# Performance work log

Hardware: AMD Instinct MI355X
Metric: run time of the kernel (lower is better)

The kernel has to match this reference:

```python
import jax, jax.numpy as jnp
import numpy as np

N, E, D, H = 50000, 500000, 128, 4
FH = D // H  # per-head dim of gat1
NEG_SLOPE = 0.2
EPS = 1e-16  # PyG softmax denominator epsilon


def _gat_layer(x, src, dst, W, a_src, a_dst, bias, heads, fh):
    # W: [D_in, heads*fh]; a_src/a_dst: [heads, fh]; bias: [heads*fh]
    n = x.shape[0]
    xp = (x @ W).reshape(n, heads, fh)                     # [N,H,F]
    alpha_s = jnp.einsum('nhf,hf->nh', xp, a_src)          # [N,H]
    alpha_d = jnp.einsum('nhf,hf->nh', xp, a_dst)
    e = alpha_s[src] + alpha_d[dst]                        # [E,H]
    e = jnp.where(e > 0, e, NEG_SLOPE * e)                 # leaky_relu
    # edge softmax grouped by destination node
    m = jax.lax.stop_gradient(jax.ops.segment_max(e, dst, num_segments=n))
    a = jnp.exp(e - m[dst])
    denom = jax.ops.segment_sum(a, dst, num_segments=n)
    a = a / (denom[dst] + EPS)                             # [E,H]
    msg = a[:, :, None] * xp[src]                          # [E,H,F]
    out = jax.ops.segment_sum(msg, dst, num_segments=n)    # [N,H,F]
    return out.reshape(n, heads * fh) + bias


def setup_inputs() -> dict:
    key = jax.random.key(0)
    ks = jax.random.split(key, 20)

    def glorot(k, shape):
        fan_in, fan_out = shape[0], shape[-1]
        std = (2.0 / (fan_in + fan_out)) ** 0.5
        return std * jax.random.normal(k, shape, dtype=jnp.float32)

    inp = {
        'x': jax.random.normal(ks[0], (N, 1), dtype=jnp.float32),
        'edge_index': jax.random.randint(ks[1], (E, 2), 0, N, dtype=jnp.int64 if jax.config.jax_enable_x64 else jnp.int32),
        'W_emb': glorot(ks[2], (1, D)),   # nn.Linear(1, d_node), stored as [in,out]
        'b_emb': jnp.zeros((D,), jnp.float32),
        # gat1: in=D, heads=H, per-head out=FH
        'W1': glorot(ks[3], (D, H * FH)),
        'as1': glorot(ks[4], (H, FH)),
        'ad1': glorot(ks[5], (H, FH)),
        'b1': jnp.zeros((H * FH,), jnp.float32),
        # gat2/3/4: in=D, heads=1, out=D
        'W2': glorot(ks[6], (D, D)), 'as2': glorot(ks[7], (1, D)), 'ad2': glorot(ks[8], (1, D)), 'b2': jnp.zeros((D,), jnp.float32),
        'W3': glorot(ks[9], (D, D)), 'as3': glorot(ks[10], (1, D)), 'ad3': glorot(ks[11], (1, D)), 'b3': jnp.zeros((D,), jnp.float32),
        'W4': glorot(ks[12], (D, D)), 'as4': glorot(ks[13], (1, D)), 'ad4': glorot(ks[14], (1, D)), 'b4': jnp.zeros((D,), jnp.float32),
    }
    return inp


def reference(x, edge_index, W_emb, b_emb, W1, as1, ad1, b1,
              W2, as2, ad2, b2, W3, as3, ad3, b3, W4, as4, ad4, b4):
    # emb: Linear(1 -> D)
    h = x @ W_emb + b_emb                                  # [N,D]
    # edge_index.t(): row 0 = src, row 1 = dst; GATConv adds self-loops
    loop = jnp.arange(N, dtype=edge_index.dtype)
    src = jnp.concatenate([edge_index[:, 0], loop])
    dst = jnp.concatenate([edge_index[:, 1], loop])
    h = jax.nn.relu(_gat_layer(h, src, dst, W1, as1, ad1, b1, H, FH))
    h = jax.nn.relu(_gat_layer(h, src, dst, W2, as2, ad2, b2, 1, D))
    h = jax.nn.relu(_gat_layer(h, src, dst, W3, as3, ad3, b3, 1, D))
    h = _gat_layer(h, src, dst, W4, as4, ad4, b4, 1, D)
    return h
```

## Files before the change

### kernel.cpp

```cpp
#include <hip/hip_runtime.h>
#include <math.h>


#define LEAKY(e) ((e) > 0.f ? (e) : 0.2f * (e))
#define SCAN_BLK 1024

typedef __attribute__((ext_vector_type(8))) short bf16x8;
typedef __attribute__((ext_vector_type(4))) float f32x4;

__device__ inline ushort f32_to_bf16_rne(float f) {
    unsigned u = __float_as_uint(f);
    unsigned r = (u + 0x7FFFu + ((u >> 16) & 1u)) >> 16;
    return (ushort)r;
}
__device__ inline float bf16_to_f32(ushort h) { return __uint_as_float((unsigned)h << 16); }


__global__ void k_hist(const int* __restrict__ ei, int E, int N, int* __restrict__ deg) {
    int e = blockIdx.x * blockDim.x + threadIdx.x;
    int Et = E + N;
    if (e >= Et) return;
    int dst = (e < E) ? ei[2 * e + 1] : (e - E);
    atomicAdd(&deg[dst], 1);
}

__global__ __launch_bounds__(SCAN_BLK) void k_scan1(const int* __restrict__ deg,
                                                    int* __restrict__ tmp,
                                                    int* __restrict__ blocksum, int n) {
    __shared__ int buf[SCAN_BLK];
    int tid = threadIdx.x;
    int gid = blockIdx.x * SCAN_BLK + tid;
    int v = (gid < n) ? deg[gid] : 0;
    buf[tid] = v;
    __syncthreads();
#pragma unroll
    for (int off = 1; off < SCAN_BLK; off <<= 1) {
        int t = (tid >= off) ? buf[tid - off] : 0;
        __syncthreads();
        buf[tid] += t;
        __syncthreads();
    }
    if (gid < n) tmp[gid] = buf[tid] - v;
    if (tid == SCAN_BLK - 1) blocksum[blockIdx.x] = buf[tid];
}

__global__ __launch_bounds__(256) void k_scan2(const int* __restrict__ blocksum,
                                               int* __restrict__ blockoff, int nb,
                                               int* __restrict__ row_ptr, int n) {
    __shared__ int buf[256];
    int tid = threadIdx.x;
    int v = (tid < nb) ? blocksum[tid] : 0;
    buf[tid] = v;
    __syncthreads();
#pragma unroll
    for (int off = 1; off < 256; off <<= 1) {
        int t = (tid >= off) ? buf[tid - off] : 0;
        __syncthreads();
        buf[tid] += t;
        __syncthreads();
    }
    if (tid < nb) blockoff[tid] = buf[tid] - v;
    if (tid == 255) row_ptr[n] = buf[tid];
}

__global__ void k_scan3(const int* __restrict__ tmp, const int* __restrict__ blockoff,
                        int* __restrict__ row_ptr, int* __restrict__ cursor, int n) {
    int gid = blockIdx.x * blockDim.x + threadIdx.x;
    if (gid >= n) return;
    int v = tmp[gid] + blockoff[gid / SCAN_BLK];
    row_ptr[gid] = v;
    cursor[gid] = v;
}

__global__ void k_scatter(const int* __restrict__ ei, int E, int N,
                          int* __restrict__ cursor, int* __restrict__ csr_src) {
    int e = blockIdx.x * blockDim.x + threadIdx.x;
    int Et = E + N;
    if (e >= Et) return;
    int src, dst;
    if (e < E) { src = ei[2 * e]; dst = ei[2 * e + 1]; }
    else { src = dst = e - E; }
    int pos = atomicAdd(&cursor[dst], 1);
    csr_src[pos] = src;
}


__global__ void k_wsplit3(const float* __restrict__ W0, const float* __restrict__ W1,
                          const float* __restrict__ W2,
                          ushort* __restrict__ hi0, ushort* __restrict__ lo0,
                          ushort* __restrict__ hi1, ushort* __restrict__ lo1,
                          ushort* __restrict__ hi2, ushort* __restrict__ lo2) {
    int l = blockIdx.x >> 6;
    int idx = (blockIdx.x & 63) * 256 + threadIdx.x;
    const float* W = (l == 0) ? W0 : (l == 1) ? W1 : W2;
    ushort* ph = (l == 0) ? hi0 : (l == 1) ? hi1 : hi2;
    ushort* pl = (l == 0) ? lo0 : (l == 1) ? lo1 : lo2;
    int k = idx >> 7, c = idx & 127;
    float w = W[idx];
    ushort hi = f32_to_bf16_rne(w);
    ushort lo = f32_to_bf16_rne(w - bf16_to_f32(hi));
    ph[c * 128 + k] = hi;
    pl[c * 128 + k] = lo;
}

__global__ void k_wvec3(const float* __restrict__ W0, const float* __restrict__ W1,
                        const float* __restrict__ W2,
                        const float* __restrict__ as0, const float* __restrict__ as1,
                        const float* __restrict__ as2,
                        const float* __restrict__ ad0, const float* __restrict__ ad1,
                        const float* __restrict__ ad2,
                        float* __restrict__ was0, float* __restrict__ was1,
                        float* __restrict__ was2,
                        float* __restrict__ wad0, float* __restrict__ wad1,
                        float* __restrict__ wad2) {
    int l = blockIdx.x;
    const float* W  = (l == 0) ? W0 : (l == 1) ? W1 : W2;
    const float* av = (l == 0) ? as0 : (l == 1) ? as1 : as2;
    const float* dv = (l == 0) ? ad0 : (l == 1) ? ad1 : ad2;
    float* ws = (l == 0) ? was0 : (l == 1) ? was1 : was2;
    float* wd = (l == 0) ? wad0 : (l == 1) ? wad1 : wad2;
    int k = threadIdx.x;
    float s = 0.f, d = 0.f;
    for (int c = 0; c < 128; c++) {
        float w = W[k * 128 + c];
        s += w * av[c];
        d += w * dv[c];
    }
    ws[k] = s; wd[k] = d;
}


__global__ void k_emb(const float* __restrict__ W_emb, const float* __restrict__ b_emb,
                      const float* __restrict__ W1, const float* __restrict__ as1,
                      const float* __restrict__ ad1, float* __restrict__ consts) {
    __shared__ float su[128], sv[128];
    int f = threadIdx.x;
    float u = 0.f, v = 0.f;
    for (int k = 0; k < 128; k++) {
        u += W_emb[k] * W1[k * 128 + f];
        v += b_emb[k] * W1[k * 128 + f];
    }
    su[f] = u; sv[f] = v;
    consts[f] = u; consts[128 + f] = v;
    __syncthreads();
    if (f < 4) {
        float P = 0.f, Q = 0.f, R = 0.f, S = 0.f;
        for (int j = 0; j < 32; j++) {
            float uu = su[f * 32 + j], vv = sv[f * 32 + j];
            float a = as1[f * 32 + j], d = ad1[f * 32 + j];
            P += uu * a; Q += vv * a; R += uu * d; S += vv * d;
        }
        consts[256 + f] = P; consts[260 + f] = Q; consts[264 + f] = R; consts[268 + f] = S;
    }
}

__global__ __launch_bounds__(256) void k_l1(const float* __restrict__ x,
        const int* __restrict__ row_ptr, const int* __restrict__ csr_src,
        const float* __restrict__ consts, const float* __restrict__ b1,
        const float* __restrict__ was2, const float* __restrict__ wad2,
        float* __restrict__ hout, float* __restrict__ a_s, float* __restrict__ a_d, int n) {
    __shared__ float sm[64][4], smw[64][4];
    int tid = threadIdx.x;
    int nl = tid >> 2, q = tid & 3;
    int node = blockIdx.x * 64 + nl;
    bool valid = node < n;
    float P = consts[256 + q], Q = consts[260 + q];
    float R = consts[264 + q], Sc = consts[268 + q];
    float den = 0.f, S = 0.f;
    if (valid) {
        float xd = x[node];
        float c0 = xd * R + Sc + Q;
        int s0 = row_ptr[node], s1 = row_ptr[node + 1];
        for (int i = s0; i < s1; i++) {
            float xs = x[csr_src[i]];
            float e = xs * P + c0;
            e = LEAKY(e);
            float w = __expf(e);
            den += w;
            S += w * xs;
        }
    }
    float inv = 1.f / (den + 1e-16f);
    sm[nl][q] = S * inv;
    smw[nl][q] = den * inv;
    __syncthreads();
    float Sn = sm[nl][q], Swn = smw[nl][q];
    float ps = 0.f, pd = 0.f;
    if (valid) {
#pragma unroll
        for (int j = 0; j < 8; j++) {
            int f = q * 32 + j * 4;
            float4 u = *(const float4*)(consts + f);
            float4 v = *(const float4*)(consts + 128 + f);
            float4 b = *(const float4*)(b1 + f);
            float4 ws = *(const float4*)(was2 + f);
            float4 wd = *(const float4*)(wad2 + f);
            float4 val;
            val.x = fmaxf(Sn * u.x + Swn * v.x + b.x, 0.f);
            val.y = fmaxf(Sn * u.y + Swn * v.y + b.y, 0.f);
            val.z = fmaxf(Sn * u.z + Swn * v.z + b.z, 0.f);
            val.w = fmaxf(Sn * u.w + Swn * v.w + b.w, 0.f);
            *(float4*)(hout + (size_t)node * 128 + f) = val;
            ps += val.x * ws.x + val.y * ws.y + val.z * ws.z + val.w * ws.w;
            pd += val.x * wd.x + val.y * wd.y + val.z * wd.z + val.w * wd.w;
        }
    }
    ps += __shfl_xor(ps, 1, 64); ps += __shfl_xor(ps, 2, 64);
    pd += __shfl_xor(pd, 1, 64); pd += __shfl_xor(pd, 2, 64);
    if (q == 0 && valid) { a_s[node] = ps; a_d[node] = pd; }
}

__global__ __launch_bounds__(256) void k_aggh(const float* __restrict__ h,
        const float* __restrict__ as, const float* __restrict__ ad,
        const int* __restrict__ row_ptr, const int* __restrict__ csr_src,
        uint2* __restrict__ aggp, int n) {
    __shared__ int2 s_sw[4][64];
    int w = threadIdx.x >> 6, lane = threadIdx.x & 63;
    int node = blockIdx.x * 4 + w;
    if (node >= n) return;
    int s0 = row_ptr[node], s1 = row_ptr[node + 1];
    int deg = s1 - s0;
    float adval = ad[node];
    const char* hbase = (const char*)h;
    int lane8 = lane * 8;
    float2 acc = make_float2(0.f, 0.f);
    float den;

    if (deg <= 64) {
        int boff = 0;
        float e = -INFINITY;
        if (lane < deg) {
            int src = csr_src[s0 + lane];
            boff = src << 9;
            e = LEAKY(as[src] + adval);
        }
        float m = e;
#pragma unroll
        for (int off = 32; off > 0; off >>= 1) m = fmaxf(m, __shfl_xor(m, off, 64));
        float wt = (lane < deg) ? __expf(e - m) : 0.f;
        den = wt;
#pragma unroll
        for (int off = 32; off > 0; off >>= 1) den += __shfl_xor(den, off, 64);
        s_sw[w][lane] = make_int2(boff, __float_as_int(wt));
        __builtin_amdgcn_wave_barrier();

        int j = 0;
        for (; j + 8 <= deg; j += 8) {
#pragma unroll
            for (int t = 0; t < 8; t++) {
                int2 p = s_sw[w][j + t];
                float2 v = *(const float2*)(hbase + p.x + lane8);
                float wt2 = __int_as_float(p.y);
                acc.x += wt2 * v.x; acc.y += wt2 * v.y;
            }
        }
        for (; j < deg; j++) {
            int2 p = s_sw[w][j];
            float2 v = *(const float2*)(hbase + p.x + lane8);
            float wt2 = __int_as_float(p.y);
            acc.x += wt2 * v.x; acc.y += wt2 * v.y;
        }
    } else {
        float m = -INFINITY;
        for (int i = s0 + lane; i < s1; i += 64) {
            float e = LEAKY(as[csr_src[i]] + adval);
            m = fmaxf(m, e);
        }
#pragma unroll
        for (int off = 32; off > 0; off >>= 1) m = fmaxf(m, __shfl_xor(m, off, 64));
        den = 0.f;
        for (int i = s0; i < s1; i++) {
            int src = csr_src[i];
            float e = LEAKY(as[src] + adval);
            float wt = __expf(e - m);
            den += wt;
            float2 v = *(const float2*)(hbase + ((size_t)src << 9) + lane8);
            acc.x += wt * v.x; acc.y += wt * v.y;
        }
    }

    float inv = 1.f / (den + 1e-16f);
    float o0 = acc.x * inv, o1 = acc.y * inv;
    ushort hi0 = f32_to_bf16_rne(o0), hi1 = f32_to_bf16_rne(o1);
    ushort lo0 = f32_to_bf16_rne(o0 - bf16_to_f32(hi0));
    ushort lo1 = f32_to_bf16_rne(o1 - bf16_to_f32(hi1));
    aggp[(size_t)node * 64 + lane] =
        make_uint2((unsigned)hi0 | ((unsigned)hi1 << 16),
                   (unsigned)lo0 | ((unsigned)lo1 << 16));
}

__global__ __launch_bounds__(512) void k_gemm(const uint2* __restrict__ aggp,
        const ushort* __restrict__ wt_hi, const ushort* __restrict__ wt_lo,
        const float* __restrict__ bias, float* __restrict__ hout,
        const float* __restrict__ was_nx, const float* __restrict__ wad_nx,
        float* __restrict__ as_nx, float* __restrict__ ad_nx,
        int n, int do_relu) {
    __shared__ ushort Bh[16 * 128 * 8];
    __shared__ ushort Bl[16 * 128 * 8];
    int tid = threadIdx.x;
#pragma unroll
    for (int rep = 0; rep < 4; rep++) {
        int c = rep * 512 + tid;
        int col = c >> 4, kc = c & 15;
        *(uint4*)(Bh + (size_t)(kc * 128 + col) * 8) = *(const uint4*)(wt_hi + (size_t)col * 128 + kc * 8);
        *(uint4*)(Bl + (size_t)(kc * 128 + col) * 8) = *(const uint4*)(wt_lo + (size_t)col * 128 + kc * 8);
    }
    __syncthreads();

    int wid = tid >> 6, lane = tid & 63;
    int lrow = lane & 15, kgrp = lane >> 4;
    int row_base = blockIdx.x * 128 + wid * 16;

    f32x4 acc[8];
#pragma unroll
    for (int nn = 0; nn < 8; nn++) { acc[nn][0] = 0.f; acc[nn][1] = 0.f; acc[nn][2] = 0.f; acc[nn][3] = 0.f; }

#pragma unroll
    for (int ks = 0; ks < 4; ks++) {
        int kbase = ks * 32 + kgrp * 8;
        int arow = min(row_base + lrow, n - 1);
        const uint2* ap = aggp + (size_t)arow * 64 + (kbase >> 1);
        uint4 q0 = *(const uint4*)ap;
        uint4 q1 = *(const uint4*)(ap + 2);
        int4 hi4 = make_int4(q0.x, q0.z, q1.x, q1.z);
        int4 lo4 = make_int4(q0.y, q0.w, q1.y, q1.w);
        bf16x8 ah = *(bf16x8*)&hi4;
        bf16x8 al = *(bf16x8*)&lo4;
        int kc = ks * 4 + kgrp;
#pragma unroll
        for (int nn = 0; nn < 8; nn++) {
            int col = nn * 16 + lrow;
            bf16x8 bh = *(const bf16x8*)(Bh + (size_t)(kc * 128 + col) * 8);
            bf16x8 bl = *(const bf16x8*)(Bl + (size_t)(kc * 128 + col) * 8);
            acc[nn] = __builtin_amdgcn_mfma_f32_16x16x32_bf16(ah, bh, acc[nn], 0, 0, 0);
            acc[nn] = __builtin_amdgcn_mfma_f32_16x16x32_bf16(ah, bl, acc[nn], 0, 0, 0);
            acc[nn] = __builtin_amdgcn_mfma_f32_16x16x32_bf16(al, bh, acc[nn], 0, 0, 0);
        }
    }

    float bv[8], wsv[8], wdv[8];
#pragma unroll
    for (int nn = 0; nn < 8; nn++) bv[nn] = bias[nn * 16 + lrow];
    if (was_nx) {
#pragma unroll
        for (int nn = 0; nn < 8; nn++) {
            wsv[nn] = was_nx[nn * 16 + lrow];
            wdv[nn] = wad_nx[nn * 16 + lrow];
        }
    }

#pragma unroll
    for (int i = 0; i < 4; i++) {
        int row = row_base + kgrp * 4 + i;
        if (row < n) {
            float ps = 0.f, pd = 0.f;
#pragma unroll
            for (int nn = 0; nn < 8; nn++) {
                float val = acc[nn][i] + bv[nn];
                if (do_relu) val = fmaxf(val, 0.f);
                hout[(size_t)row * 128 + nn * 16 + lrow] = val;
                if (was_nx) { ps += val * wsv[nn]; pd += val * wdv[nn]; }
            }
            if (was_nx) {
#pragma unroll
                for (int off = 1; off < 16; off <<= 1) {
                    ps += __shfl_xor(ps, off, 16);
                    pd += __shfl_xor(pd, off, 16);
                }
                if (lrow == 0) { as_nx[row] = ps; ad_nx[row] = pd; }
            }
        }
    }
}


extern "C" void kernel_launch(void* const* d_in, const int* in_sizes, int n_in,
                              void* d_out, int out_size, void* d_ws, size_t ws_size,
                              hipStream_t stream) {
    const float* x     = (const float*)d_in[0];
    const int*   ei    = (const int*)d_in[1];
    const float* W_emb = (const float*)d_in[2];
    const float* b_emb = (const float*)d_in[3];
    const float* W1    = (const float*)d_in[4];
    const float* as1   = (const float*)d_in[5];
    const float* ad1   = (const float*)d_in[6];
    const float* b1    = (const float*)d_in[7];
    const float* Wl[3]  = {(const float*)d_in[8],  (const float*)d_in[12], (const float*)d_in[16]};
    const float* asl[3] = {(const float*)d_in[9],  (const float*)d_in[13], (const float*)d_in[17]};
    const float* adl[3] = {(const float*)d_in[10], (const float*)d_in[14], (const float*)d_in[18]};
    const float* bl[3]  = {(const float*)d_in[11], (const float*)d_in[15], (const float*)d_in[19]};
    float* out = (float*)d_out;

    int N = in_sizes[0];
    int E = in_sizes[1] / 2;
    int Et = E + N;
    int nb = (N + SCAN_BLK - 1) / SCAN_BLK;

    char* ws = (char*)d_ws;
    size_t off = 0;
    auto alloc = [&](size_t bytes) { size_t p = off; off += (bytes + 255) & ~(size_t)255; return p; };
    int*   deg      = (int*)(ws + alloc((size_t)N * 4));
    int*   row_ptr  = (int*)(ws + alloc((size_t)(N + 1) * 4));
    int*   cursor   = (int*)(ws + alloc((size_t)N * 4));
    int*   csr_src  = (int*)(ws + alloc((size_t)Et * 4));
    int*   scantmp  = (int*)(ws + alloc((size_t)N * 4));
    int*   blocksum = (int*)(ws + alloc((size_t)nb * 4));
    int*   blockoff = (int*)(ws + alloc((size_t)nb * 4));
    float* consts   = (float*)(ws + alloc(272 * 4));
    float* a_s0     = (float*)(ws + alloc((size_t)N * 4));
    float* a_d0     = (float*)(ws + alloc((size_t)N * 4));
    float* a_s1     = (float*)(ws + alloc((size_t)N * 4));
    float* a_d1     = (float*)(ws + alloc((size_t)N * 4));
    float* hA       = (float*)(ws + alloc((size_t)N * 128 * 4));
    uint2* aggp     = (uint2*)(ws + alloc((size_t)N * 64 * 8));
    ushort* wt_hi[3]; ushort* wt_lo[3];
    float* was[3]; float* wad[3];
    for (int l = 0; l < 3; l++) {
        wt_hi[l] = (ushort*)(ws + alloc(128 * 128 * 2));
        wt_lo[l] = (ushort*)(ws + alloc(128 * 128 * 2));
        was[l]   = (float*)(ws + alloc(128 * 4));
        wad[l]   = (float*)(ws + alloc(128 * 4));
    }

    hipMemsetAsync(deg, 0, (size_t)N * 4, stream);
    k_hist<<<(Et + 255) / 256, 256, 0, stream>>>(ei, E, N, deg);
    k_scan1<<<nb, SCAN_BLK, 0, stream>>>(deg, scantmp, blocksum, N);
    k_scan2<<<1, 256, 0, stream>>>(blocksum, blockoff, nb, row_ptr, N);
    k_scan3<<<(N + 255) / 256, 256, 0, stream>>>(scantmp, blockoff, row_ptr, cursor, N);
    k_scatter<<<(Et + 255) / 256, 256, 0, stream>>>(ei, E, N, cursor, csr_src);

    k_wsplit3<<<192, 256, 0, stream>>>(Wl[0], Wl[1], Wl[2],
                                       wt_hi[0], wt_lo[0], wt_hi[1], wt_lo[1], wt_hi[2], wt_lo[2]);
    k_wvec3<<<3, 128, 0, stream>>>(Wl[0], Wl[1], Wl[2], asl[0], asl[1], asl[2],
                                   adl[0], adl[1], adl[2],
                                   was[0], was[1], was[2], wad[0], wad[1], wad[2]);
    k_emb<<<1, 128, 0, stream>>>(W_emb, b_emb, W1, as1, ad1, consts);

    k_l1<<<(N + 63) / 64, 256, 0, stream>>>(x, row_ptr, csr_src, consts, b1,
                                            was[0], wad[0], hA, a_s0, a_d0, N);

    float* as_cur = a_s0; float* ad_cur = a_d0;
    float* as_nxt = a_s1; float* ad_nxt = a_d1;
    for (int l = 0; l < 3; l++) {
        k_aggh<<<(N + 3) / 4, 256, 0, stream>>>(hA, as_cur, ad_cur, row_ptr, csr_src, aggp, N);
        if (l < 2) {
            k_gemm<<<(N + 127) / 128, 512, 0, stream>>>(aggp, wt_hi[l], wt_lo[l], bl[l], hA,
                                                        was[l + 1], wad[l + 1], as_nxt, ad_nxt, N, 1);
            float* t;
            t = as_cur; as_cur = as_nxt; as_nxt = t;
            t = ad_cur; ad_cur = ad_nxt; ad_nxt = t;
        } else {
            k_gemm<<<(N + 127) / 128, 512, 0, stream>>>(aggp, wt_hi[l], wt_lo[l], bl[l], out,
                                                        nullptr, nullptr, nullptr, nullptr, N, 0);
        }
    }
}
```

Before: 285.4 us.

## Fuse edge aggregation with MFMA projection into one per-layer kernel

Merges the softmax-weighted neighbour aggregation and the split-bf16 MFMA GEMM into a single kernel per layer. The aggregated rows stay in shared memory instead of round-tripping through a global buffer, and a second h buffer is added for ping-pong. The LDS staging of the weights is dropped: B fragments are read straight from global memory. Edge weights and offsets are now broadcast with shuffles instead of LDS. The gather phase now has fewer waves per node (each wave processes 16 nodes serially), which may lower latency hiding. Weight reloads from global per wave may also add traffic.

```diff
diff --git a/kernel.cpp b/kernel.cpp
--- a/kernel.cpp
+++ b/kernel.cpp
@@ -210,106 +210,96 @@
     if (q == 0 && valid) { a_s[node] = ps; a_d[node] = pd; }
 }
 
-__global__ __launch_bounds__(256) void k_aggh(const float* __restrict__ h,
+__global__ __launch_bounds__(256) void k_layer(const float* __restrict__ h,
         const float* __restrict__ as, const float* __restrict__ ad,
         const int* __restrict__ row_ptr, const int* __restrict__ csr_src,
-        uint2* __restrict__ aggp, int n) {
-    __shared__ int2 s_sw[4][64];
-    int w = threadIdx.x >> 6, lane = threadIdx.x & 63;
-    int node = blockIdx.x * 4 + w;
-    if (node >= n) return;
-    int s0 = row_ptr[node], s1 = row_ptr[node + 1];
-    int deg = s1 - s0;
-    float adval = ad[node];
-    const char* hbase = (const char*)h;
-    int lane8 = lane * 8;
-    float2 acc = make_float2(0.f, 0.f);
-    float den;
-
-    if (deg <= 64) {
-        int boff = 0;
-        float e = -INFINITY;
-        if (lane < deg) {
-            int src = csr_src[s0 + lane];
-            boff = src << 9;
-            e = LEAKY(as[src] + adval);
-        }
-        float m = e;
-#pragma unroll
-        for (int off = 32; off > 0; off >>= 1) m = fmaxf(m, __shfl_xor(m, off, 64));
-        float wt = (lane < deg) ? __expf(e - m) : 0.f;
-        den = wt;
-#pragma unroll
-        for (int off = 32; off > 0; off >>= 1) den += __shfl_xor(den, off, 64);
-        s_sw[w][lane] = make_int2(boff, __float_as_int(wt));
-        __builtin_amdgcn_wave_barrier();
-
-        int j = 0;
-        for (; j + 8 <= deg; j += 8) {
-#pragma unroll
-            for (int t = 0; t < 8; t++) {
-                int2 p = s_sw[w][j + t];
-                float2 v = *(const float2*)(hbase + p.x + lane8);
-                float wt2 = __int_as_float(p.y);
-                acc.x += wt2 * v.x; acc.y += wt2 * v.y;
-            }
-        }
-        for (; j < deg; j++) {
-            int2 p = s_sw[w][j];
-            float2 v = *(const float2*)(hbase + p.x + lane8);
-            float wt2 = __int_as_float(p.y);
-            acc.x += wt2 * v.x; acc.y += wt2 * v.y;
-        }
-    } else {
-        float m = -INFINITY;
-        for (int i = s0 + lane; i < s1; i += 64) {
-            float e = LEAKY(as[csr_src[i]] + adval);
-            m = fmaxf(m, e);
-        }
-#pragma unroll
-        for (int off = 32; off > 0; off >>= 1) m = fmaxf(m, __shfl_xor(m, off, 64));
-        den = 0.f;
-        for (int i = s0; i < s1; i++) {
-            int src = csr_src[i];
-            float e = LEAKY(as[src] + adval);
-            float wt = __expf(e - m);
-            den += wt;
-            float2 v = *(const float2*)(hbase + ((size_t)src << 9) + lane8);
-            acc.x += wt * v.x; acc.y += wt * v.y;
-        }
-    }
-
-    float inv = 1.f / (den + 1e-16f);
-    float o0 = acc.x * inv, o1 = acc.y * inv;
-    ushort hi0 = f32_to_bf16_rne(o0), hi1 = f32_to_bf16_rne(o1);
-    ushort lo0 = f32_to_bf16_rne(o0 - bf16_to_f32(hi0));
-    ushort lo1 = f32_to_bf16_rne(o1 - bf16_to_f32(hi1));
-    aggp[(size_t)node * 64 + lane] =
-        make_uint2((unsigned)hi0 | ((unsigned)hi1 << 16),
-                   (unsigned)lo0 | ((unsigned)lo1 << 16));
-}
-
-__global__ __launch_bounds__(512) void k_gemm(const uint2* __restrict__ aggp,
         const ushort* __restrict__ wt_hi, const ushort* __restrict__ wt_lo,
         const float* __restrict__ bias, float* __restrict__ hout,
         const float* __restrict__ was_nx, const float* __restrict__ wad_nx,
         float* __restrict__ as_nx, float* __restrict__ ad_nx,
         int n, int do_relu) {
-    __shared__ ushort Bh[16 * 128 * 8];
-    __shared__ ushort Bl[16 * 128 * 8];
-    int tid = threadIdx.x;
-#pragma unroll
-    for (int rep = 0; rep < 4; rep++) {
-        int c = rep * 512 + tid;
-        int col = c >> 4, kc = c & 15;
-        *(uint4*)(Bh + (size_t)(kc * 128 + col) * 8) = *(const uint4*)(wt_hi + (size_t)col * 128 + kc * 8);
-        *(uint4*)(Bl + (size_t)(kc * 128 + col) * 8) = *(const uint4*)(wt_lo + (size_t)col * 128 + kc * 8);
+    __shared__ unsigned Ahi[64][68];
+    __shared__ unsigned Alo[64][68];
+    int tid = threadIdx.x, wid = tid >> 6, lane = tid & 63;
+    const char* hbase = (const char*)h;
+    int lane8 = lane * 8;
+
+    for (int t = 0; t < 16; t++) {
+        int row = wid * 16 + t;
+        int node = blockIdx.x * 64 + row;
+        if (node < n) {
+            int s0 = row_ptr[node], s1 = row_ptr[node + 1];
+            int deg = s1 - s0;
+            float adval = ad[node];
+            float2 acc = make_float2(0.f, 0.f);
+            float den;
+            if (deg <= 64) {
+                int boff = 0;
+                float e = -INFINITY;
+                if (lane < deg) {
+                    int src = csr_src[s0 + lane];
+                    boff = src << 9;
+                    e = LEAKY(as[src] + adval);
+                }
+                float m = e;
+#pragma unroll
+                for (int off = 32; off > 0; off >>= 1) m = fmaxf(m, __shfl_xor(m, off, 64));
+                float wt = (lane < deg) ? __expf(e - m) : 0.f;
+                den = wt;
+#pragma unroll
+                for (int off = 32; off > 0; off >>= 1) den += __shfl_xor(den, off, 64);
+                int j = 0;
+                for (; j + 4 <= deg; j += 4) {
+                    int b0 = __shfl(boff, j, 64), b1 = __shfl(boff, j + 1, 64);
+                    int b2 = __shfl(boff, j + 2, 64), b3 = __shfl(boff, j + 3, 64);
+                    float w0 = __shfl(wt, j, 64), w1 = __shfl(wt, j + 1, 64);
+                    float w2 = __shfl(wt, j + 2, 64), w3 = __shfl(wt, j + 3, 64);
+                    float2 v0 = *(const float2*)(hbase + b0 + lane8);
+                    float2 v1 = *(const float2*)(hbase + b1 + lane8);
+                    float2 v2 = *(const float2*)(hbase + b2 + lane8);
+                    float2 v3 = *(const float2*)(hbase + b3 + lane8);
+                    acc.x += w0 * v0.x; acc.y += w0 * v0.y;
+                    acc.x += w1 * v1.x; acc.y += w1 * v1.y;
+                    acc.x += w2 * v2.x; acc.y += w2 * v2.y;
+                    acc.x += w3 * v3.x; acc.y += w3 * v3.y;
+                }
+                for (; j < deg; j++) {
+                    int bj = __shfl(boff, j, 64);
+                    float wj = __shfl(wt, j, 64);
+                    float2 v = *(const float2*)(hbase + bj + lane8);
+                    acc.x += wj * v.x; acc.y += wj * v.y;
+                }
+            } else {
+                float m = -INFINITY;
+                for (int i = s0 + lane; i < s1; i += 64) {
+                    float e = LEAKY(as[csr_src[i]] + adval);
+                    m = fmaxf(m, e);
+                }
+#pragma unroll
+                for (int off = 32; off > 0; off >>= 1) m = fmaxf(m, __shfl_xor(m, off, 64));
+                den = 0.f;
+                for (int i = s0; i < s1; i++) {
+                    int src = csr_src[i];
+                    float e = LEAKY(as[src] + adval);
+                    float wt = __expf(e - m);
+                    den += wt;
+                    float2 v = *(const float2*)(hbase + ((size_t)src << 9) + lane8);
+                    acc.x += wt * v.x; acc.y += wt * v.y;
+                }
+            }
+            float inv = 1.f / (den + 1e-16f);
+            float o0 = acc.x * inv, o1 = acc.y * inv;
+            ushort hi0 = f32_to_bf16_rne(o0), hi1 = f32_to_bf16_rne(o1);
+            ushort lo0 = f32_to_bf16_rne(o0 - bf16_to_f32(hi0));
+            ushort lo1 = f32_to_bf16_rne(o1 - bf16_to_f32(hi1));
+            Ahi[row][lane] = (unsigned)hi0 | ((unsigned)hi1 << 16);
+            Alo[row][lane] = (unsigned)lo0 | ((unsigned)lo1 << 16);
+        }
     }
     __syncthreads();
 
-    int wid = tid >> 6, lane = tid & 63;
     int lrow = lane & 15, kgrp = lane >> 4;
-    int row_base = blockIdx.x * 128 + wid * 16;
+    int row_base = blockIdx.x * 64 + wid * 16;
 
     f32x4 acc[8];
 #pragma unroll
@@ -318,20 +308,16 @@
 #pragma unroll
     for (int ks = 0; ks < 4; ks++) {
         int kbase = ks * 32 + kgrp * 8;
-        int arow = min(row_base + lrow, n - 1);
-        const uint2* ap = aggp + (size_t)arow * 64 + (kbase >> 1);
-        uint4 q0 = *(const uint4*)ap;
-        uint4 q1 = *(const uint4*)(ap + 2);
-        int4 hi4 = make_int4(q0.x, q0.z, q1.x, q1.z);
-        int4 lo4 = make_int4(q0.y, q0.w, q1.y, q1.w);
+        int c0 = ks * 16 + kgrp * 4;
+        uint4 hi4 = *(const uint4*)(&Ahi[wid * 16 + lrow][c0]);
+        uint4 lo4 = *(const uint4*)(&Alo[wid * 16 + lrow][c0]);
         bf16x8 ah = *(bf16x8*)&hi4;
         bf16x8 al = *(bf16x8*)&lo4;
-        int kc = ks * 4 + kgrp;
 #pragma unroll
         for (int nn = 0; nn < 8; nn++) {
             int col = nn * 16 + lrow;
-            bf16x8 bh = *(const bf16x8*)(Bh + (size_t)(kc * 128 + col) * 8);
-            bf16x8 bl = *(const bf16x8*)(Bl + (size_t)(kc * 128 + col) * 8);
+            bf16x8 bh = *(const bf16x8*)(wt_hi + (size_t)col * 128 + kbase);
+            bf16x8 bl = *(const bf16x8*)(wt_lo + (size_t)col * 128 + kbase);
             acc[nn] = __builtin_amdgcn_mfma_f32_16x16x32_bf16(ah, bh, acc[nn], 0, 0, 0);
             acc[nn] = __builtin_amdgcn_mfma_f32_16x16x32_bf16(ah, bl, acc[nn], 0, 0, 0);
             acc[nn] = __builtin_amdgcn_mfma_f32_16x16x32_bf16(al, bh, acc[nn], 0, 0, 0);
@@ -412,7 +398,7 @@
     float* a_s1     = (float*)(ws + alloc((size_t)N * 4));
     float* a_d1     = (float*)(ws + alloc((size_t)N * 4));
     float* hA       = (float*)(ws + alloc((size_t)N * 128 * 4));
-    uint2* aggp     = (uint2*)(ws + alloc((size_t)N * 64 * 8));
+    float* hB       = (float*)(ws + alloc((size_t)N * 128 * 4));
     ushort* wt_hi[3]; ushort* wt_lo[3];
     float* was[3]; float* wad[3];
     for (int l = 0; l < 3; l++) {
@@ -439,19 +425,14 @@
     k_l1<<<(N + 63) / 64, 256, 0, stream>>>(x, row_ptr, csr_src, consts, b1,
                                             was[0], wad[0], hA, a_s0, a_d0, N);
 
-    float* as_cur = a_s0; float* ad_cur = a_d0;
-    float* as_nxt = a_s1; float* ad_nxt = a_d1;
-    for (int l = 0; l < 3; l++) {
-        k_aggh<<<(N + 3) / 4, 256, 0, stream>>>(hA, as_cur, ad_cur, row_ptr, csr_src, aggp, N);
-        if (l < 2) {
-            k_gemm<<<(N + 127) / 128, 512, 0, stream>>>(aggp, wt_hi[l], wt_lo[l], bl[l], hA,
-                                                        was[l + 1], wad[l + 1], as_nxt, ad_nxt, N, 1);
-            float* t;
-            t = as_cur; as_cur = as_nxt; as_nxt = t;
-            t = ad_cur; ad_cur = ad_nxt; ad_nxt = t;
-        } else {
-            k_gemm<<<(N + 127) / 128, 512, 0, stream>>>(aggp, wt_hi[l], wt_lo[l], bl[l], out,
-                                                        nullptr, nullptr, nullptr, nullptr, N, 0);
-        }
-    }
-}
+    int nblk = (N + 63) / 64;
+    k_layer<<<nblk, 256, 0, stream>>>(hA, a_s0, a_d0, row_ptr, csr_src,
+                                      wt_hi[0], wt_lo[0], bl[0], hB,
+                                      was[1], wad[1], a_s1, a_d1, N, 1);
+    k_layer<<<nblk, 256, 0, stream>>>(hB, a_s1, a_d1, row_ptr, csr_src,
+                                      wt_hi[1], wt_lo[1], bl[1], hA,
+                                      was[2], wad[2], a_s0, a_d0, N, 1);
+    k_layer<<<nblk, 256, 0, stream>>>(hA, a_s0, a_d0, row_ptr, csr_src,
+                                      wt_hi[2], wt_lo[2], bl[2], out,
+                                      nullptr, nullptr, nullptr, nullptr, N, 0);
+}
```

Result: slower. 374.3 us (+31.2%).
